# Optimization experiments

Hardware: AMD Instinct MI355X
Metric: run time of the kernel (lower is better)

## Reference

```python
import jax, jax.numpy as jnp
import numpy as np

S, B, D, H = 512, 32, 1024, 1024

def setup_inputs() -> dict:
    key = jax.random.key(0)
    ks = jax.random.split(key, 7)
    return {
        "layer_input": jax.random.normal(ks[0], (S, B, D), dtype=jnp.float32),
        "h_t": jax.random.normal(ks[1], (B, H), dtype=jnp.float32),
        "c_t": jax.random.normal(ks[2], (B, H), dtype=jnp.float32),
        "U": jax.random.normal(ks[3], (4 * H, D), dtype=jnp.float32) * 0.05,
        "V": jax.random.normal(ks[4], (4 * H, H), dtype=jnp.float32) * 0.05,
        "bih": jax.random.normal(ks[5], (4 * H,), dtype=jnp.float32) * 0.05,
        "bhh": jax.random.normal(ks[6], (4 * H,), dtype=jnp.float32) * 0.05,
    }


def reference(layer_input, h_t, c_t, U, V, bih, bhh):
    # hard=False, quantize=False, rw_dropout=0 => standard LSTM recurrence
    Ut = U.T  # [D, 4H]
    Vt = V.T  # [H, 4H]
    bias = bih + bhh  # [4H]

    def step(carry, x_t):
        h, c = carry
        gates = x_t @ Ut + h @ Vt + bias  # [B, 4H]
        i, f, g, o = jnp.split(gates, 4, axis=1)
        i = jax.nn.sigmoid(i)
        f = jax.nn.sigmoid(f)
        g = jnp.tanh(g)
        o = jax.nn.sigmoid(o)
        c_new = f * c + i * g
        h_new = o * jnp.tanh(c_new)
        return (h_new, c_new), (h_new, c_new)

    (h_f, c_f), (all_h, all_c) = jax.lax.scan(step, (h_t, c_t), layer_input)
    # torch returns (output, (h_t, c_t), (all_h, all_c)); output == all_h
    return (all_h, h_f, c_f, all_h, all_c)
```

## Files before the change

### kernel.cpp

```cpp
#include <hip/hip_runtime.h>

#define S_LEN 512
#define B_SZ  32
#define H_SZ  1024
#define NG    4096
#define K_SZ  1024
#define GWG   128
#define PWG   96

typedef __attribute__((ext_vector_type(8))) short short8;
typedef __attribute__((ext_vector_type(4))) float floatx4;
typedef __attribute__((ext_vector_type(4))) unsigned short ushort4v;

__device__ __forceinline__ unsigned short f2bf(float f){
  unsigned u = __float_as_uint(f);
  u += 0x7fffu + ((u >> 16) & 1u);
  return (unsigned short)(u >> 16);
}
__device__ __forceinline__ float bf2f(unsigned short u){
  return __uint_as_float(((unsigned)u) << 16);
}
__device__ __forceinline__ float sigm(float x){ return 1.f / (1.f + __expf(-x)); }
__device__ __forceinline__ float tanh_f(float x){
  float ax = fabsf(x);
  float e = __expf(-2.f * ax);
  float r = (1.f - e) / (1.f + e);
  return copysignf(r, x);
}

__global__ __launch_bounds__(256) void cvt_bf16(const float* __restrict__ s,
                                                unsigned short* __restrict__ d, int n){
  int i = (blockIdx.x * 256 + threadIdx.x) * 4;
  if (i < n){
    float4 v = *(const float4*)(s + i);
    ushort4v o; o.x = f2bf(v.x); o.y = f2bf(v.y); o.z = f2bf(v.z); o.w = f2bf(v.w);
    *(ushort4v*)(d + i) = o;
  }
}

__global__ __launch_bounds__(256) void cvt_h0(const float* __restrict__ s,
                                              unsigned short* __restrict__ d,
                                              unsigned* __restrict__ flags){
  int i = (blockIdx.x * 256 + threadIdx.x) * 4;
  float4 v = *(const float4*)(s + i);
  ushort4v o; o.x = f2bf(v.x); o.y = f2bf(v.y); o.z = f2bf(v.z); o.w = f2bf(v.w);
  *(ushort4v*)(d + i) = o;
  if (blockIdx.x == 0){
    flags[threadIdx.x] = 0u;
    flags[256 + threadIdx.x] = 0u;
    flags[512 + threadIdx.x] = 0u;
  }
}

#define LPAD 1032
#define GPADW 36
__global__ __launch_bounds__(256) void fused(const short* __restrict__ Xb,
                                             const short* __restrict__ Ub,
                                             unsigned short* __restrict__ gates_pre,
                                             const short* __restrict__ Vb,
                                             const float* __restrict__ bih,
                                             const float* __restrict__ bhh,
                                             const float* __restrict__ c0,
                                             unsigned short* __restrict__ hh,
                                             unsigned* __restrict__ flags,
                                             unsigned* __restrict__ gp_cnt,
                                             float* __restrict__ out){
  __shared__ alignas(16) char smem[136704];
  const int tid = threadIdx.x;
  const int wave = tid >> 6, lane = tid & 63;
  const int ml = lane & 15, lg = lane >> 4;

  if (blockIdx.x >= GWG){
    short* As = (short*)smem;
    short* Bs = (short*)(smem + 8192);
    const int g = blockIdx.x - GWG;
    const int wm = (wave >> 1) * 64, wn = (wave & 1) * 64;
    for (int item = g; item < 4096; item += PWG){
      const int bm = item >> 5, bn = item & 31;
      floatx4 acc[4][4] = {};
      const short* Abase = Xb + (size_t)bm * 128 * K_SZ;
      const short* Bbase = Ub + (size_t)bn * 128 * K_SZ;
      for (int k0 = 0; k0 < K_SZ; k0 += 32){
#pragma unroll
        for (int i = 0; i < 2; ++i){
          int r0 = (wave * 2 + i) * 16;
          int row = r0 + (lane >> 2);
          int cof = (lane & 3) * 8;
          __builtin_amdgcn_global_load_lds(
            (const __attribute__((address_space(1))) void*)(Abase + (size_t)row * K_SZ + k0 + cof),
            (__attribute__((address_space(3))) void*)(As + r0 * 32), 16, 0, 0);
          __builtin_amdgcn_global_load_lds(
            (const __attribute__((address_space(1))) void*)(Bbase + (size_t)row * K_SZ + k0 + cof),
            (__attribute__((address_space(3))) void*)(Bs + r0 * 32), 16, 0, 0);
        }
        __syncthreads();
        short8 af[4], bf[4];
#pragma unroll
        for (int mt = 0; mt < 4; ++mt) af[mt] = *(const short8*)&As[(wm + mt * 16 + ml) * 32 + lg * 8];
#pragma unroll
        for (int nt = 0; nt < 4; ++nt) bf[nt] = *(const short8*)&Bs[(wn + nt * 16 + ml) * 32 + lg * 8];
#pragma unroll
        for (int mt = 0; mt < 4; ++mt)
#pragma unroll
          for (int nt = 0; nt < 4; ++nt)
            acc[mt][nt] = __builtin_amdgcn_mfma_f32_16x16x32_bf16(af[mt], bf[nt], acc[mt][nt], 0, 0, 0);
        __syncthreads();
      }
#pragma unroll
      for (int mt = 0; mt < 4; ++mt){
#pragma unroll
        for (int nt = 0; nt < 4; ++nt){
          const int row0 = bm * 128 + wm + mt * 16 + lg * 4;
          const int col  = bn * 128 + wn + nt * 16 + ml;
#pragma unroll
          for (int r = 0; r < 4; ++r)
            __hip_atomic_store(&gates_pre[(size_t)(row0 + r) * NG + col],
                               f2bf(acc[mt][nt][r]),
                               __ATOMIC_RELAXED, __HIP_MEMORY_SCOPE_AGENT);
        }
      }
      asm volatile("s_waitcnt vmcnt(0)" ::: "memory");
      __syncthreads();
      if (tid == 0)
        __hip_atomic_fetch_add(gp_cnt + bm, 1u, __ATOMIC_RELAXED, __HIP_MEMORY_SCOPE_AGENT);
    }
    return;
  }

  short* Vs = (short*)smem;
  short* hS = (short*)(smem + 66048);
  float* gatesS = (float*)(smem + 132096);

  const int wg = blockIdx.x;
  const int j0 = wg * 8;
  const int mt = wave >> 1, nt = wave & 1;

#pragma unroll
  for (int i = 0; i < 16; ++i){
    int e = i * 2048 + tid * 8;
    int rr = e >> 10, cc = e & 1023;
    int gg = rr >> 3, rloc = rr & 7;
    const short* src = Vb + (size_t)(gg * 1024 + j0 + rloc) * 1024 + cc;
    *(short8*)&Vs[rr * LPAD + cc] = *(const short8*)src;
  }
  const int b_own = tid >> 3, jj_own = tid & 7;
  float bias_i = bih[0 * 1024 + j0 + jj_own] + bhh[0 * 1024 + j0 + jj_own];
  float bias_f = bih[1 * 1024 + j0 + jj_own] + bhh[1 * 1024 + j0 + jj_own];
  float bias_g = bih[2 * 1024 + j0 + jj_own] + bhh[2 * 1024 + j0 + jj_own];
  float bias_o = bih[3 * 1024 + j0 + jj_own] + bhh[3 * 1024 + j0 + jj_own];
  float c_reg  = c0[b_own * 1024 + j0 + jj_own];
  __syncthreads();

  const size_t SBH = (size_t)S_LEN * B_SZ * H_SZ;
  const size_t BH  = (size_t)B_SZ * H_SZ;
  float* out_h  = out;
  float* out_hf = out + SBH;
  float* out_cf = out + SBH + BH;
  float* out_h2 = out + SBH + 2 * BH;
  float* out_c  = out + 2 * SBH + 2 * BH;

  const int c_sl = nt * 16 + ml;
  const int gcol = (c_sl >> 3) * 1024 + j0 + (c_sl & 7);

  while (__hip_atomic_load(gp_cnt, __ATOMIC_RELAXED, __HIP_MEMORY_SCOPE_AGENT) < 32u)
    __builtin_amdgcn_s_sleep(2);
  unsigned ready_hi = 0;

  unsigned short gpr0, gpr1, gpr2, gpr3;
  {
    const unsigned short* gp = gates_pre + (size_t)(0 * 32 + mt * 16 + lg * 4) * NG + gcol;
    gpr0 = gp[0]; gpr1 = gp[NG]; gpr2 = gp[2 * (size_t)NG]; gpr3 = gp[3 * (size_t)NG];
  }

  for (int t = 0; t < S_LEN; ++t){
    if (t > 0){
      if (tid < 128){
        const unsigned* f = flags + tid * 4;
        while (__hip_atomic_load(f, __ATOMIC_RELAXED, __HIP_MEMORY_SCOPE_AGENT) < (unsigned)t)
          __builtin_amdgcn_s_sleep(1);
      }
      __syncthreads();
    }
    const unsigned want = (unsigned)(t >> 2) + 1u;
    const bool do_probe = (want < 128u) && (want > ready_hi);
    unsigned probev = 0;
    if (do_probe)
      probev = __hip_atomic_load(gp_cnt + want, __ATOMIC_RELAXED, __HIP_MEMORY_SCOPE_AGENT);
    const unsigned short* hb = hh + (size_t)t * 32768;
#pragma unroll
    for (int i = 0; i < 16; ++i){
      int e_base = i * 2048 + wave * 512;
      int rr = e_base >> 10, cc0 = e_base & 1023;
      __builtin_amdgcn_global_load_lds(
        (const __attribute__((address_space(1))) void*)(hb + e_base + lane * 8),
        (__attribute__((address_space(3))) void*)(hS + rr * LPAD + cc0), 16, 0, 17);
    }
    floatx4 acc0, acc1;
    acc0[0] = bf2f(gpr0); acc0[1] = bf2f(gpr1); acc0[2] = bf2f(gpr2); acc0[3] = bf2f(gpr3);
    acc1[0] = 0.f; acc1[1] = 0.f; acc1[2] = 0.f; acc1[3] = 0.f;
    __syncthreads();
    const int abase = (mt * 16 + ml) * LPAD + lg * 8;
    const int bbase = (nt * 16 + ml) * LPAD + lg * 8;
#pragma unroll
    for (int kk = 0; kk < 32; kk += 2){
      short8 a0 = *(const short8*)&hS[abase + kk * 32];
      short8 b0 = *(const short8*)&Vs[bbase + kk * 32];
      short8 a1 = *(const short8*)&hS[abase + kk * 32 + 32];
      short8 b1 = *(const short8*)&Vs[bbase + kk * 32 + 32];
      acc0 = __builtin_amdgcn_mfma_f32_16x16x32_bf16(a0, b0, acc0, 0, 0, 0);
      acc1 = __builtin_amdgcn_mfma_f32_16x16x32_bf16(a1, b1, acc1, 0, 0, 0);
    }
    acc0 += acc1;
#pragma unroll
    for (int r = 0; r < 4; ++r)
      gatesS[(mt * 16 + lg * 4 + r) * GPADW + c_sl] = acc0[r];
    __syncthreads();
    float hv, cv;
    {
      float gi = gatesS[b_own * GPADW + jj_own]      + bias_i;
      float gf = gatesS[b_own * GPADW + 8 + jj_own]  + bias_f;
      float gg = gatesS[b_own * GPADW + 16 + jj_own] + bias_g;
      float go = gatesS[b_own * GPADW + 24 + jj_own] + bias_o;
      float iv = sigm(gi), fv = sigm(gf), gv = tanh_f(gg), ov = sigm(go);
      cv = fv * c_reg + iv * gv;
      c_reg = cv;
      hv = ov * tanh_f(cv);
    }
    if (t + 1 < S_LEN){
      unsigned u  = (unsigned)f2bf(hv);
      unsigned n1 = __shfl_down(u, 1);
      unsigned p  = u | (n1 << 16);
      unsigned p2 = __shfl_down(p, 2);
      if ((tid & 3) == 0){
        unsigned long long v = (unsigned long long)p | ((unsigned long long)p2 << 32);
        unsigned long long* dst =
          (unsigned long long*)(hh + (size_t)(t + 1) * 32768 + (size_t)b_own * 1024 + j0 + jj_own);
        __hip_atomic_store(dst, v, __ATOMIC_RELAXED, __HIP_MEMORY_SCOPE_AGENT);
      }
      asm volatile("s_waitcnt vmcnt(0)" ::: "memory");
      __syncthreads();
      if (tid == 0)
        __hip_atomic_store(flags + wg * 4, (unsigned)(t + 1),
                           __ATOMIC_RELAXED, __HIP_MEMORY_SCOPE_AGENT);
      if (do_probe && probev >= 32u) ready_hi = want;
      const unsigned bmn = (unsigned)(t + 1) >> 2;
      if (bmn > ready_hi){
        while (__hip_atomic_load(gp_cnt + bmn, __ATOMIC_RELAXED, __HIP_MEMORY_SCOPE_AGENT) < 32u)
          __builtin_amdgcn_s_sleep(1);
        ready_hi = bmn;
      }
      const unsigned short* gp = gates_pre + (size_t)((t + 1) * 32 + mt * 16 + lg * 4) * NG + gcol;
      gpr0 = gp[0]; gpr1 = gp[NG]; gpr2 = gp[2 * (size_t)NG]; gpr3 = gp[3 * (size_t)NG];
    }
    {
      size_t o = (size_t)t * BH + (size_t)b_own * H_SZ + (size_t)(j0 + jj_own);
      out_h[o]  = hv;
      out_h2[o] = hv;
      out_c[o]  = cv;
      if (t == S_LEN - 1){
        out_hf[b_own * H_SZ + j0 + jj_own] = hv;
        out_cf[b_own * H_SZ + j0 + jj_own] = cv;
      }
    }
  }
}

#define WS_FLG 0
#define WS_HH  4096
#define WS_XB  (4096 + 513 * 65536)
#define WS_UB  (WS_XB + 33554432)
#define WS_VB  (WS_UB + 8388608)
#define WS_GP  (WS_VB + 8388608)

extern "C" void kernel_launch(void* const* d_in, const int* in_sizes, int n_in,
                              void* d_out, int out_size, void* d_ws, size_t ws_size,
                              hipStream_t stream) {
  const float* X   = (const float*)d_in[0];
  const float* h0  = (const float*)d_in[1];
  const float* c0  = (const float*)d_in[2];
  const float* U   = (const float*)d_in[3];
  const float* V   = (const float*)d_in[4];
  const float* bih = (const float*)d_in[5];
  const float* bhh = (const float*)d_in[6];
  float* out = (float*)d_out;
  char* ws = (char*)d_ws;

  unsigned* flags      = (unsigned*)(ws + WS_FLG);
  unsigned* gp_cnt     = (unsigned*)(ws + WS_FLG + 2048);
  unsigned short* hh   = (unsigned short*)(ws + WS_HH);
  unsigned short* Xb   = (unsigned short*)(ws + WS_XB);
  unsigned short* Ub   = (unsigned short*)(ws + WS_UB);
  unsigned short* Vb   = (unsigned short*)(ws + WS_VB);
  unsigned short* gates = (unsigned short*)(ws + WS_GP);

  cvt_bf16<<<dim3(16384), 256, 0, stream>>>(X, Xb, 16777216);
  cvt_bf16<<<dim3(4096),  256, 0, stream>>>(U, Ub, 4194304);
  cvt_bf16<<<dim3(4096),  256, 0, stream>>>(V, Vb, 4194304);
  cvt_h0  <<<dim3(32),    256, 0, stream>>>(h0, hh, flags);
  fused   <<<dim3(GWG + PWG), 256, 0, stream>>>((const short*)Xb, (const short*)Ub, gates,
                                                (const short*)Vb, bih, bhh, c0,
                                                hh, flags, gp_cnt, out);
}
```

Before: 2.555 ms.

## Replace per-step flag barrier with sentinel-polled hidden state data

Removes the per-workgroup step flags and their store-then-poll handshake. The h buffer is pre-filled with a NaN sentinel, and consumers atomically poll the h data itself until no sentinel remains, then write it to LDS. This drops one round-trip of flag publish, the vmcnt wait and a syncthreads per step. In exchange it adds a fill kernel, uses many registers for the 32 polled values, and depends on no real bf16 output matching the sentinel pattern.

```diff
diff --git a/kernel.cpp b/kernel.cpp
--- a/kernel.cpp
+++ b/kernel.cpp
@@ -7,10 +7,12 @@
 #define K_SZ  1024
 #define GWG   128
 #define PWG   96
+#define SENT32 0xFFC0FFC0u
 
 typedef __attribute__((ext_vector_type(8))) short short8;
 typedef __attribute__((ext_vector_type(4))) float floatx4;
 typedef __attribute__((ext_vector_type(4))) unsigned short ushort4v;
+typedef __attribute__((ext_vector_type(4))) unsigned int uintx4;
 
 __device__ __forceinline__ unsigned short f2bf(float f){
   unsigned u = __float_as_uint(f);
@@ -36,6 +38,12 @@
     ushort4v o; o.x = f2bf(v.x); o.y = f2bf(v.y); o.z = f2bf(v.z); o.w = f2bf(v.w);
     *(ushort4v*)(d + i) = o;
   }
+}
+
+__global__ __launch_bounds__(256) void fill_sent(unsigned short* __restrict__ hh){
+  size_t i = 32768 + ((size_t)blockIdx.x * 256 + threadIdx.x) * 8;
+  uintx4 v; v[0] = SENT32; v[1] = SENT32; v[2] = SENT32; v[3] = SENT32;
+  *(uintx4*)(hh + i) = v;
 }
 
 __global__ __launch_bounds__(256) void cvt_h0(const float* __restrict__ s,
@@ -46,8 +54,6 @@
   ushort4v o; o.x = f2bf(v.x); o.y = f2bf(v.y); o.z = f2bf(v.z); o.w = f2bf(v.w);
   *(ushort4v*)(d + i) = o;
   if (blockIdx.x == 0){
-    flags[threadIdx.x] = 0u;
-    flags[256 + threadIdx.x] = 0u;
     flags[512 + threadIdx.x] = 0u;
   }
 }
@@ -62,7 +68,6 @@
                                              const float* __restrict__ bhh,
                                              const float* __restrict__ c0,
                                              unsigned short* __restrict__ hh,
-                                             unsigned* __restrict__ flags,
                                              unsigned* __restrict__ gp_cnt,
                                              float* __restrict__ out){
   __shared__ alignas(16) char smem[136704];
@@ -173,27 +178,42 @@
   }
 
   for (int t = 0; t < S_LEN; ++t){
-    if (t > 0){
-      if (tid < 128){
-        const unsigned* f = flags + tid * 4;
-        while (__hip_atomic_load(f, __ATOMIC_RELAXED, __HIP_MEMORY_SCOPE_AGENT) < (unsigned)t)
-          __builtin_amdgcn_s_sleep(1);
-      }
-      __syncthreads();
-    }
     const unsigned want = (unsigned)(t >> 2) + 1u;
     const bool do_probe = (want < 128u) && (want > ready_hi);
     unsigned probev = 0;
     if (do_probe)
       probev = __hip_atomic_load(gp_cnt + want, __ATOMIC_RELAXED, __HIP_MEMORY_SCOPE_AGENT);
-    const unsigned short* hb = hh + (size_t)t * 32768;
-#pragma unroll
-    for (int i = 0; i < 16; ++i){
-      int e_base = i * 2048 + wave * 512;
-      int rr = e_base >> 10, cc0 = e_base & 1023;
-      __builtin_amdgcn_global_load_lds(
-        (const __attribute__((address_space(1))) void*)(hb + e_base + lane * 8),
-        (__attribute__((address_space(3))) void*)(hS + rr * LPAD + cc0), 16, 0, 17);
+
+    {
+      const unsigned short* hb = hh + (size_t)t * 32768;
+      const unsigned long long* Pq =
+        (const unsigned long long*)(hb + wave * 512 + lane * 8);
+      unsigned long long r[32];
+      unsigned pend = 0xFFFFFFFFu;
+      do {
+#pragma unroll
+        for (int s = 0; s < 32; ++s)
+          if (pend & (1u << s))
+            r[s] = __hip_atomic_load(Pq + (s >> 1) * 512 + (s & 1),
+                                     __ATOMIC_RELAXED, __HIP_MEMORY_SCOPE_AGENT);
+        unsigned np = 0;
+#pragma unroll
+        for (int s = 0; s < 32; ++s)
+          if (pend & (1u << s)){
+            unsigned lo = (unsigned)r[s], hi = (unsigned)(r[s] >> 32);
+            if (lo == SENT32 || hi == SENT32) np |= (1u << s);
+          }
+        pend = np;
+      } while (__any(pend != 0));
+#pragma unroll
+      for (int i = 0; i < 16; ++i){
+        int g = i * 2048 + wave * 512 + lane * 8;
+        int rr = g >> 10, cc = g & 1023;
+        unsigned long long a = r[2 * i], b = r[2 * i + 1];
+        uintx4 v; v[0] = (unsigned)a; v[1] = (unsigned)(a >> 32);
+        v[2] = (unsigned)b; v[3] = (unsigned)(b >> 32);
+        *(uintx4*)&hS[rr * LPAD + cc] = v;
+      }
     }
     floatx4 acc0, acc1;
     acc0[0] = bf2f(gpr0); acc0[1] = bf2f(gpr1); acc0[2] = bf2f(gpr2); acc0[3] = bf2f(gpr3);
@@ -237,11 +257,6 @@
           (unsigned long long*)(hh + (size_t)(t + 1) * 32768 + (size_t)b_own * 1024 + j0 + jj_own);
         __hip_atomic_store(dst, v, __ATOMIC_RELAXED, __HIP_MEMORY_SCOPE_AGENT);
       }
-      asm volatile("s_waitcnt vmcnt(0)" ::: "memory");
-      __syncthreads();
-      if (tid == 0)
-        __hip_atomic_store(flags + wg * 4, (unsigned)(t + 1),
-                           __ATOMIC_RELAXED, __HIP_MEMORY_SCOPE_AGENT);
       if (do_probe && probev >= 32u) ready_hi = want;
       const unsigned bmn = (unsigned)(t + 1) >> 2;
       if (bmn > ready_hi){
@@ -293,11 +308,12 @@
   unsigned short* Vb   = (unsigned short*)(ws + WS_VB);
   unsigned short* gates = (unsigned short*)(ws + WS_GP);
 
-  cvt_bf16<<<dim3(16384), 256, 0, stream>>>(X, Xb, 16777216);
-  cvt_bf16<<<dim3(4096),  256, 0, stream>>>(U, Ub, 4194304);
-  cvt_bf16<<<dim3(4096),  256, 0, stream>>>(V, Vb, 4194304);
-  cvt_h0  <<<dim3(32),    256, 0, stream>>>(h0, hh, flags);
-  fused   <<<dim3(GWG + PWG), 256, 0, stream>>>((const short*)Xb, (const short*)Ub, gates,
-                                                (const short*)Vb, bih, bhh, c0,
-                                                hh, flags, gp_cnt, out);
-}
+  cvt_bf16 <<<dim3(16384), 256, 0, stream>>>(X, Xb, 16777216);
+  cvt_bf16 <<<dim3(4096),  256, 0, stream>>>(U, Ub, 4194304);
+  cvt_bf16 <<<dim3(4096),  256, 0, stream>>>(V, Vb, 4194304);
+  fill_sent<<<dim3(8192),  256, 0, stream>>>(hh);
+  cvt_h0   <<<dim3(32),    256, 0, stream>>>(h0, hh, flags);
+  fused    <<<dim3(GWG + PWG), 256, 0, stream>>>((const short*)Xb, (const short*)Ub, gates,
+                                                 (const short*)Vb, bih, bhh, c0,
+                                                 hh, gp_cnt, out);
+}
```

Result: slower. 3.269 ms (+27.9%).
